# Performance work log

Hardware: AMD Instinct MI355X
Metric: run time of the kernel (lower is better)

The kernel has to match this reference:

```python
import jax, jax.numpy as jnp
import numpy as np
import math

B, T, DM = 2, 2048, 2048
H, D = 16, 128
HALF = D // 2


def _rope_tables(T, half, base=10000.0):
    inv_freq = 1.0 / (base ** (np.arange(0, half, dtype=np.float32) / half))
    t = np.arange(T, dtype=np.float32)
    freqs = np.outer(t, inv_freq)  # [T, half]
    return jnp.asarray(np.cos(freqs)), jnp.asarray(np.sin(freqs))


def setup_inputs() -> dict:
    key = jax.random.key(0)
    ks = jax.random.split(key, 5)
    s = 1.0 / math.sqrt(DM)
    x = jax.random.normal(ks[0], (B, T, DM), dtype=jnp.float32)
    wq = jax.random.normal(ks[1], (H * D, DM), dtype=jnp.float32) * s
    wk = jax.random.normal(ks[2], (H * D, DM), dtype=jnp.float32) * s
    wv = jax.random.normal(ks[3], (H * D, DM), dtype=jnp.float32) * s
    wo = jax.random.normal(ks[4], (DM, H * D), dtype=jnp.float32) * s
    cos, sin = _rope_tables(T, HALF)
    return {"x": x, "wq": wq, "wk": wk, "wv": wv, "wo": wo, "cos": cos, "sin": sin}


def _apply_rope(x, cos, sin):
    # x: [B,H,T,D]; cos/sin: [T, D//2] broadcast over batch and head
    x1, x2 = x[..., :HALF], x[..., HALF:]
    c = cos[None, None]
    s = sin[None, None]
    return jnp.concatenate([x1 * c - x2 * s, x1 * s + x2 * c], axis=-1)


def reference(x, wq, wk, wv, wo, cos, sin):
    Bx, Tx, _ = x.shape
    # QKV projections (Linear with weight [out,in]): y = x @ W^T
    q = jnp.einsum('btd,ed->bte', x, wq).reshape(Bx, Tx, H, D).transpose(0, 2, 1, 3)
    k = jnp.einsum('btd,ed->bte', x, wk).reshape(Bx, Tx, H, D).transpose(0, 2, 1, 3)
    v = jnp.einsum('btd,ed->bte', x, wv).reshape(Bx, Tx, H, D).transpose(0, 2, 1, 3)
    q = _apply_rope(q, cos, sin)
    k = _apply_rope(k, cos, sin)
    # causal SDPA (prefill path: kv_cache=None, mask='causal')
    scale = 1.0 / math.sqrt(D)
    scores = jnp.einsum('bhqd,bhkd->bhqk', q, k) * scale  # [B,H,T,T]
    causal = jnp.tril(jnp.ones((Tx, Tx), dtype=bool))
    scores = jnp.where(causal[None, None], scores, jnp.finfo(scores.dtype).min)
    attn = jax.nn.softmax(scores, axis=-1)
    out = jnp.einsum('bhqk,bhkd->bhqd', attn, v)  # [B,H,T,D]
    out = out.transpose(0, 2, 1, 3).reshape(Bx, Tx, H * D)
    return jnp.einsum('bte,de->btd', out, wo)
```

## Files before the change

### kernel.cpp

```cpp
#include <hip/hip_runtime.h>

typedef __attribute__((ext_vector_type(8))) short short8;
typedef __attribute__((ext_vector_type(4))) float floatx4;

#define B_ 2
#define T_ 2048
#define DM_ 2048
#define H_ 16
#define D_ 128
#define HALF_ 64

__device__ inline unsigned short f2bf(float f) {
    union { float f; unsigned u; } v; v.f = f;
    unsigned r = (v.u + 0x7fffu + ((v.u >> 16) & 1u)) >> 16;
    return (unsigned short)r;
}

__device__ inline void gld16(const void* g, void* l) {
    __builtin_amdgcn_global_load_lds(
        (__attribute__((address_space(1))) void*)g,
        (__attribute__((address_space(3))) void*)l,
        16, 0, 0);
}

__global__ void conv_all(const float* __restrict__ x,
                         const float* __restrict__ w0, const float* __restrict__ w1,
                         const float* __restrict__ w2, const float* __restrict__ w3,
                         unsigned short* __restrict__ xb,
                         unsigned short* __restrict__ wb, int n4w) {
    int y = blockIdx.y;
    int i = blockIdx.x * 256 + threadIdx.x;
    const float* src;
    ushort4* dst;
    if (y < 2) { src = x + (size_t)y * n4w * 4; dst = (ushort4*)xb + (size_t)y * n4w; }
    else {
        src = (y == 2) ? w0 : (y == 3) ? w1 : (y == 4) ? w2 : w3;
        dst = (ushort4*)wb + (size_t)(y - 2) * n4w;
    }
    float4 f = ((const float4*)src)[i];
    ushort4 o;
    o.x = f2bf(f.x); o.y = f2bf(f.y); o.z = f2bf(f.z); o.w = f2bf(f.w);
    dst[i] = o;
}

__global__ __launch_bounds__(256)
void gemm_qkv(const unsigned short* __restrict__ A,
              const unsigned short* __restrict__ W,
              unsigned short* __restrict__ q,
              unsigned short* __restrict__ k,
              unsigned short* __restrict__ vt,
              const float* __restrict__ cosT,
              const float* __restrict__ sinT) {
    __shared__ unsigned short sh[18432];
    unsigned short* As = sh;
    unsigned short* Bs = sh + 8192;

    const int t    = threadIdx.x;
    const int lane = t & 63;
    const int w    = t >> 6;
    const int wm   = w >> 1, wn = w & 1;
    const int l15  = lane & 15, quad = lane >> 4;
    const int bx   = blockIdx.x;
    const int row0 = blockIdx.y * 128;
    const int colg0 = bx * 128;
    const int h     = bx & 15;
    const int K = DM_;

    floatx4 acc[4][4];
    for (int i = 0; i < 4; ++i)
        for (int j = 0; j < 4; ++j)
            acc[i][j] = (floatx4){0.f, 0.f, 0.f, 0.f};

    for (int kt = 0; kt < K / 64; ++kt) {
        if (kt) __syncthreads();
        for (int i = 0; i < 4; ++i) {
            int g  = i * 256 + t;
            int g0 = i * 256 + (t & ~63);
            int m  = g >> 3, c = g & 7;
            int k8 = c ^ (m & 7);
            gld16(A + (size_t)(row0 + m) * K + kt * 64 + k8 * 8, As + (size_t)g0 * 8);
            gld16(W + (size_t)(colg0 + m) * K + kt * 64 + k8 * 8, Bs + (size_t)g0 * 8);
        }
        __syncthreads();

        for (int s = 0; s < 2; ++s) {
            short8 a[4], b[4];
            for (int mf = 0; mf < 4; ++mf) {
                int row = wm * 64 + mf * 16 + l15;
                int pc  = (quad + s * 4) ^ (row & 7);
                a[mf] = *(const short8*)(As + row * 64 + pc * 8);
            }
            for (int nf = 0; nf < 4; ++nf) {
                int row = wn * 32 + (nf & 1) * 16 + (nf >> 1) * 64 + l15;
                int pc  = (quad + s * 4) ^ (row & 7);
                b[nf] = *(const short8*)(Bs + row * 64 + pc * 8);
            }
            for (int mf = 0; mf < 4; ++mf)
                for (int nf = 0; nf < 4; ++nf)
                    acc[mf][nf] = __builtin_amdgcn_mfma_f32_16x16x32_bf16(
                        a[mf], b[nf], acc[mf][nf], 0, 0, 0);
        }
    }

    if (bx < 32) {
        unsigned short* C = (bx < 16) ? q : k;
        for (int mf = 0; mf < 4; ++mf) {
            for (int nf = 0; nf < 2; ++nf) {
                int dh = wn * 32 + nf * 16 + l15;
                for (int r = 0; r < 4; ++r) {
                    int rowg = row0 + wm * 64 + mf * 16 + quad * 4 + r;
                    int tt = rowg & 2047;
                    float c = cosT[tt * 64 + dh];
                    float s = sinT[tt * 64 + dh];
                    float x1 = acc[mf][nf][r];
                    float x2 = acc[mf][nf + 2][r];
                    size_t base = (size_t)rowg * DM_ + h * D_ + dh;
                    C[base]         = f2bf(x1 * c - x2 * s);
                    C[base + HALF_] = f2bf(x1 * s + x2 * c);
                }
            }
        }
    } else {
        __syncthreads();
        unsigned short* P = sh + w * 4608;
        for (int mf = 0; mf < 4; ++mf)
            for (int nf = 0; nf < 4; ++nf) {
                int lc = nf * 16 + l15;
                ushort4 o4;
                o4.x = f2bf(acc[mf][nf][0]); o4.y = f2bf(acc[mf][nf][1]);
                o4.z = f2bf(acc[mf][nf][2]); o4.w = f2bf(acc[mf][nf][3]);
                *(ushort4*)(P + lc * 72 + mf * 16 + quad * 4) = o4;
            }
        __syncthreads();
        const int b  = row0 >> 11;
        const int t0 = (row0 & 2047) + wm * 64;
        for (int it = 0; it < 8; ++it) {
            int cidx = it * 64 + lane;
            int lc = cidx >> 3, t8 = cidx & 7;
            int dh = wn * 32 + ((lc >> 4) & 1) * 16 + (lc >> 5) * 64 + (lc & 15);
            uint4 d = *(const uint4*)(P + lc * 72 + t8 * 8);
            *(uint4*)(vt + ((size_t)(b * 16 + h) * 128 + dh) * T_ + t0 + t8 * 8) = d;
        }
    }
}

__global__ __launch_bounds__(256)
void gemm_bt(const unsigned short* __restrict__ A,
             const unsigned short* __restrict__ W,
             float* __restrict__ C, int M, int N, int K) {
    __shared__ unsigned short As[128 * 64];
    __shared__ unsigned short Bs[128 * 64];

    const int t    = threadIdx.x;
    const int lane = t & 63;
    const int w    = t >> 6;
    const int wm   = w >> 1, wn = w & 1;
    const int l15  = lane & 15, quad = lane >> 4;
    const int row0 = blockIdx.y * 128, col0 = blockIdx.x * 128;

    floatx4 acc[4][4];
    for (int i = 0; i < 4; ++i)
        for (int j = 0; j < 4; ++j)
            acc[i][j] = (floatx4){0.f, 0.f, 0.f, 0.f};

    const int nkt = K >> 6;
    for (int kt = 0; kt < nkt; ++kt) {
        if (kt) __syncthreads();
        for (int i = 0; i < 4; ++i) {
            int g  = i * 256 + t;
            int g0 = i * 256 + (t & ~63);
            int m  = g >> 3, c = g & 7;
            int k8 = c ^ (m & 7);
            gld16(A + (size_t)(row0 + m) * K + kt * 64 + k8 * 8,
                  (unsigned short*)As + (size_t)g0 * 8);
            gld16(W + (size_t)(col0 + m) * K + kt * 64 + k8 * 8,
                  (unsigned short*)Bs + (size_t)g0 * 8);
        }
        __syncthreads();

        for (int s = 0; s < 2; ++s) {
            short8 a[4], b[4];
            for (int mf = 0; mf < 4; ++mf) {
                int row = wm * 64 + mf * 16 + l15;
                int pc  = (quad + s * 4) ^ (row & 7);
                a[mf] = *(const short8*)(As + row * 64 + pc * 8);
            }
            for (int nf = 0; nf < 4; ++nf) {
                int row = wn * 64 + nf * 16 + l15;
                int pc  = (quad + s * 4) ^ (row & 7);
                b[nf] = *(const short8*)(Bs + row * 64 + pc * 8);
            }
            for (int mf = 0; mf < 4; ++mf)
                for (int nf = 0; nf < 4; ++nf)
                    acc[mf][nf] = __builtin_amdgcn_mfma_f32_16x16x32_bf16(
                        a[mf], b[nf], acc[mf][nf], 0, 0, 0);
        }
    }

    for (int mf = 0; mf < 4; ++mf)
        for (int nf = 0; nf < 4; ++nf)
            for (int r = 0; r < 4; ++r) {
                int row = row0 + wm * 64 + mf * 16 + quad * 4 + r;
                int col = col0 + wn * 64 + nf * 16 + l15;
                C[(size_t)row * N + col] = acc[mf][nf][r];
            }
}

__global__ __launch_bounds__(256)
void attn_kernel(const unsigned short* __restrict__ q,
                 const unsigned short* __restrict__ k,
                 const unsigned short* __restrict__ vt,
                 unsigned short* __restrict__ ao) {
    __shared__ unsigned short Ks[64 * 128];
    __shared__ unsigned short Vts[128 * 64];
    __shared__ unsigned short Pw[4][16 * 72];

    const int t    = threadIdx.x;
    const int lane = t & 63, w = t >> 6;
    const int l15  = lane & 15, quad = lane >> 4;
    const int j    = blockIdx.x;
    const int bh   = blockIdx.y;
    const int b    = bh >> 4, h = bh & 15;
    const int qt[2] = {31 - j, j};

    const size_t hoff  = (size_t)h * D_;
    const size_t bbase = (size_t)b * T_ * DM_;

    short8 qa[2][4];
    for (int rs = 0; rs < 2; ++rs) {
        const int qw = qt[rs] * 64 + w * 16;
        const unsigned short* qp = q + bbase + (size_t)(qw + l15) * DM_ + hoff + quad * 8;
        for (int ds = 0; ds < 4; ++ds)
            qa[rs][ds] = *(const short8*)(qp + ds * 32);
    }

    floatx4 o[2][8];
    floatx4 lacc[2];
    for (int rs = 0; rs < 2; ++rs) {
        for (int c = 0; c < 8; ++c) o[rs][c] = (floatx4){0.f, 0.f, 0.f, 0.f};
        lacc[rs] = (floatx4){0.f, 0.f, 0.f, 0.f};
    }
    const unsigned short one_bf = 0x3F80;
    short8 ones;
    for (int i = 0; i < 8; ++i) ones[i] = (short)one_bf;

    const float kS = 0.08838834764831845f;
    const int ktend = qt[0];

    for (int kt = 0; kt <= ktend; ++kt) {
        if (kt) __syncthreads();
        for (int i = 0; i < 4; ++i) {
            int it = w * 4 + i;
            int krow = it * 4 + (lane >> 4);
            int gck  = ((lane & 15) ^ (krow & 7));
            gld16(k + bbase + (size_t)(kt * 64 + krow) * DM_ + hoff + gck * 8,
                  (unsigned short*)Ks + it * 512);
            int vrow = it * 8 + (lane >> 3);
            int gcv  = ((lane & 7) ^ (vrow & 7));
            gld16(vt + ((size_t)bh * 128 + vrow) * T_ + kt * 64 + gcv * 8,
                  (unsigned short*)Vts + it * 512);
        }
        __syncthreads();

        for (int rs = 0; rs < 2; ++rs) {
            const int kd = qt[rs];
            if (kt > kd) continue;
            const int qw = qt[rs] * 64 + w * 16;

            floatx4 s[4];
            for (int f = 0; f < 4; ++f) s[f] = (floatx4){0.f, 0.f, 0.f, 0.f};
            for (int ds = 0; ds < 4; ++ds)
                for (int f = 0; f < 4; ++f) {
                    int krow = f * 16 + l15;
                    int phys = (ds * 4 + quad) ^ (krow & 7);
                    short8 bf = *(const short8*)(Ks + krow * 128 + phys * 8);
                    s[f] = __builtin_amdgcn_mfma_f32_16x16x32_bf16(qa[rs][ds], bf, s[f], 0, 0, 0);
                }

            const bool diag = (kt == kd);
            for (int r = 0; r < 4; ++r) {
                int qrow = qw + quad * 4 + r;
                for (int f = 0; f < 4; ++f) {
                    float x = s[f][r] * kS;
                    float e = __expf(x);
                    if (diag && (kt * 64 + f * 16 + l15 > qrow)) e = 0.f;
                    Pw[w][(quad * 4 + r) * 72 + f * 16 + l15] = f2bf(e);
                }
            }

            short8 pa0 = *(const short8*)(&Pw[w][l15 * 72 + quad * 8]);
            short8 pa1 = *(const short8*)(&Pw[w][l15 * 72 + 32 + quad * 8]);
            lacc[rs] = __builtin_amdgcn_mfma_f32_16x16x32_bf16(pa0, ones, lacc[rs], 0, 0, 0);
            lacc[rs] = __builtin_amdgcn_mfma_f32_16x16x32_bf16(pa1, ones, lacc[rs], 0, 0, 0);
            for (int c = 0; c < 8; ++c) {
                int vrow = c * 16 + l15;
                short8 b0 = *(const short8*)(Vts + vrow * 64 + ((quad) ^ (vrow & 7)) * 8);
                short8 b1 = *(const short8*)(Vts + vrow * 64 + ((4 + quad) ^ (vrow & 7)) * 8);
                o[rs][c] = __builtin_amdgcn_mfma_f32_16x16x32_bf16(pa0, b0, o[rs][c], 0, 0, 0);
                o[rs][c] = __builtin_amdgcn_mfma_f32_16x16x32_bf16(pa1, b1, o[rs][c], 0, 0, 0);
            }
        }
    }

    for (int rs = 0; rs < 2; ++rs) {
        const int qw = qt[rs] * 64 + w * 16;
        for (int r = 0; r < 4; ++r) {
            float inv = 1.0f / lacc[rs][r];
            int qrow = qw + quad * 4 + r;
            size_t obase = bbase + (size_t)qrow * DM_ + hoff;
            for (int c = 0; c < 8; ++c)
                ao[obase + c * 16 + l15] = f2bf(o[rs][c][r] * inv);
        }
    }
}

extern "C" void kernel_launch(void* const* d_in, const int* in_sizes, int n_in,
                              void* d_out, int out_size, void* d_ws, size_t ws_size,
                              hipStream_t stream) {
    const float* x    = (const float*)d_in[0];
    const float* wq   = (const float*)d_in[1];
    const float* wk   = (const float*)d_in[2];
    const float* wv   = (const float*)d_in[3];
    const float* wo   = (const float*)d_in[4];
    const float* cosT = (const float*)d_in[5];
    const float* sinT = (const float*)d_in[6];
    float* out = (float*)d_out;

    const size_t NX = (size_t)B_ * T_ * DM_;
    const size_t NW = (size_t)DM_ * DM_;

    unsigned short* xb  = (unsigned short*)d_ws;
    unsigned short* wqb = xb + NX;
    unsigned short* wob = wqb + 3 * NW;
    unsigned short* qb  = wob + NW;
    unsigned short* kb  = qb + NX;
    unsigned short* vtb = kb + NX;
    unsigned short* aob = vtb + NX;

    conv_all<<<dim3((int)(NW / 4 / 256), 6), 256, 0, stream>>>(
        x, wq, wk, wv, wo, xb, wqb, (int)(NW / 4));

    gemm_qkv<<<dim3(48, 32), 256, 0, stream>>>(xb, wqb, qb, kb, vtb, cosT, sinT);

    attn_kernel<<<dim3(16, B_ * H_), 256, 0, stream>>>(qb, kb, vtb, aob);

    gemm_bt<<<dim3(16, 32), 256, 0, stream>>>(aob, wob, out, B_ * T_, DM_, DM_);
}
```

Before: 356.1 us.

## Rework QKV GEMM into 256x256 tiles with double-buffered phased pipeline

The QKV projection GEMM moves from 128x128 tiles with 256 threads to 256x256 tiles with 512 threads. It double-buffers LDS via direct global-to-LDS loads, interleaving next-tile staging with four MFMA phases per k-step, using explicit barriers, waitcnt and setprio. The goal is to hide global-load latency and raise data reuse per tile. The V-transpose epilogue is rewritten with an XOR-swizzled LDS layout. Costs are a larger LDS footprint (128KB) and fewer blocks (384 vs 1536), which can hurt wave occupancy and tail balance.

New measurement: 375.0 us. +5.3%, slower.

```diff
diff --git a/kernel.cpp b/kernel.cpp
--- a/kernel.cpp
+++ b/kernel.cpp
@@ -43,7 +43,38 @@
     dst[i] = o;
 }
 
-__global__ __launch_bounds__(256)
+
+#define STG(dstoff, srcp, grow0, ii)                                        \
+    { int g_ = (ii) * 512 + t; int m_ = g_ >> 3, c_ = g_ & 7;               \
+      int k8_ = c_ ^ (m_ & 7);                                              \
+      gld16((srcp) + (size_t)((grow0) + m_) * K + (size_t)ktn * 64 + k8_ * 8, \
+            sh + (dstoff) + ((ii) * 512 + (t & ~63)) * 8); }
+
+#define DS_A(PH)                                                            \
+    { _Pragma("unroll") for (int j = 0; j < 2; ++j) {                       \
+        int row_ = (2 * (PH) + j) * 16 + l15;                               \
+        _Pragma("unroll") for (int s = 0; s < 2; ++s) {                     \
+            int pc_ = (quad + s * 4) ^ (row_ & 7);                          \
+            a[j][s] = *(const short8*)(sh + aoff + row_ * 64 + pc_ * 8); } } }
+
+#define MM(PH)                                                              \
+    { _Pragma("unroll") for (int j = 0; j < 2; ++j)                         \
+      _Pragma("unroll") for (int nf = 0; nf < 4; ++nf)                      \
+      _Pragma("unroll") for (int s = 0; s < 2; ++s)                         \
+        acc[2 * (PH) + j][nf] = __builtin_amdgcn_mfma_f32_16x16x32_bf16(    \
+            a[j][s], b[nf][s], acc[2 * (PH) + j][nf], 0, 0, 0); }
+
+#define PHASE_MID()                                                         \
+    __builtin_amdgcn_s_barrier();                                           \
+    asm volatile("s_waitcnt lgkmcnt(0)" ::: "memory");                      \
+    __builtin_amdgcn_sched_barrier(0);                                      \
+    __builtin_amdgcn_s_setprio(1);
+
+#define PHASE_END()                                                         \
+    __builtin_amdgcn_s_setprio(0);                                          \
+    __builtin_amdgcn_s_barrier();
+
+__global__ __launch_bounds__(512, 2)
 void gemm_qkv(const unsigned short* __restrict__ A,
               const unsigned short* __restrict__ W,
               unsigned short* __restrict__ q,
@@ -51,95 +82,143 @@
               unsigned short* __restrict__ vt,
               const float* __restrict__ cosT,
               const float* __restrict__ sinT) {
-    __shared__ unsigned short sh[18432];
-    unsigned short* As = sh;
-    unsigned short* Bs = sh + 8192;
+    __shared__ unsigned short sh[65536];
 
     const int t    = threadIdx.x;
     const int lane = t & 63;
     const int w    = t >> 6;
-    const int wm   = w >> 1, wn = w & 1;
+    const int wm   = w >> 2;
+    const int wn   = w & 3;
+    const int bh   = wn >> 1;
+    const int wodd = wn & 1;
     const int l15  = lane & 15, quad = lane >> 4;
     const int bx   = blockIdx.x;
-    const int row0 = blockIdx.y * 128;
-    const int colg0 = bx * 128;
-    const int h     = bx & 15;
-    const int K = DM_;
-
-    floatx4 acc[4][4];
-    for (int i = 0; i < 4; ++i)
+    const int row0 = blockIdx.y * 256;
+    const int col0 = bx * 256;
+    const int K    = DM_;
+
+    floatx4 acc[8][4];
+#pragma unroll
+    for (int i = 0; i < 8; ++i)
+#pragma unroll
         for (int j = 0; j < 4; ++j)
             acc[i][j] = (floatx4){0.f, 0.f, 0.f, 0.f};
 
-    for (int kt = 0; kt < K / 64; ++kt) {
-        if (kt) __syncthreads();
-        for (int i = 0; i < 4; ++i) {
-            int g  = i * 256 + t;
-            int g0 = i * 256 + (t & ~63);
-            int m  = g >> 3, c = g & 7;
-            int k8 = c ^ (m & 7);
-            gld16(A + (size_t)(row0 + m) * K + kt * 64 + k8 * 8, As + (size_t)g0 * 8);
-            gld16(W + (size_t)(colg0 + m) * K + kt * 64 + k8 * 8, Bs + (size_t)g0 * 8);
-        }
-        __syncthreads();
-
-        for (int s = 0; s < 2; ++s) {
-            short8 a[4], b[4];
-            for (int mf = 0; mf < 4; ++mf) {
-                int row = wm * 64 + mf * 16 + l15;
-                int pc  = (quad + s * 4) ^ (row & 7);
-                a[mf] = *(const short8*)(As + row * 64 + pc * 8);
-            }
-            for (int nf = 0; nf < 4; ++nf) {
-                int row = wn * 32 + (nf & 1) * 16 + (nf >> 1) * 64 + l15;
-                int pc  = (quad + s * 4) ^ (row & 7);
-                b[nf] = *(const short8*)(Bs + row * 64 + pc * 8);
-            }
-            for (int mf = 0; mf < 4; ++mf)
-                for (int nf = 0; nf < 4; ++nf)
-                    acc[mf][nf] = __builtin_amdgcn_mfma_f32_16x16x32_bf16(
-                        a[mf], b[nf], acc[mf][nf], 0, 0, 0);
-        }
-    }
-
-    if (bx < 32) {
-        unsigned short* C = (bx < 16) ? q : k;
-        for (int mf = 0; mf < 4; ++mf) {
+    {
+        const int ktn = 0;
+        STG(32768,        W, col0,       0);
+        STG(32768,        W, col0,       1);
+        STG(32768 + 8192, W, col0 + 128, 0);
+        STG(32768 + 8192, W, col0 + 128, 1);
+        STG(0,            A, row0,       0);
+        STG(8192,         A, row0 + 128, 0);
+        STG(0,            A, row0,       1);
+        STG(8192,         A, row0 + 128, 1);
+    }
+    asm volatile("s_waitcnt vmcnt(2)" ::: "memory");
+    __builtin_amdgcn_s_barrier();
+
+    for (int kt = 0; kt < 32; ++kt) {
+        const int cb   = kt & 1, nb = cb ^ 1;
+        const int ktn  = (kt < 31) ? kt + 1 : 31;
+        const int aoff = cb * 16384 + wm * 8192;
+        const int boff = 32768 + cb * 16384 + bh * 8192;
+        const int nbA  = nb * 16384;
+        const int nbB  = 32768 + nb * 16384;
+        short8 a[2][2];
+        short8 b[4][2];
+
+#pragma unroll
+        for (int nf = 0; nf < 4; ++nf) {
+            int lc = wodd * 32 + (nf & 1) * 16 + (nf >> 1) * 64 + l15;
+#pragma unroll
+            for (int s = 0; s < 2; ++s) {
+                int pc = (quad + s * 4) ^ (lc & 7);
+                b[nf][s] = *(const short8*)(sh + boff + lc * 64 + pc * 8);
+            }
+        }
+        DS_A(0)
+        STG(nbB, W, col0, 0);
+        STG(nbB, W, col0, 1);
+        PHASE_MID()
+        MM(0)
+        PHASE_END()
+
+        DS_A(1)
+        STG(nbB + 8192, W, col0 + 128, 0);
+        STG(nbB + 8192, W, col0 + 128, 1);
+        PHASE_MID()
+        MM(1)
+        __builtin_amdgcn_s_setprio(0);
+        asm volatile("s_waitcnt vmcnt(4)" ::: "memory");
+        __builtin_amdgcn_s_barrier();
+
+        DS_A(2)
+        STG(nbA,        A, row0,       0);
+        STG(nbA + 8192, A, row0 + 128, 0);
+        PHASE_MID()
+        MM(2)
+        PHASE_END()
+
+        DS_A(3)
+        STG(nbA,        A, row0,       1);
+        STG(nbA + 8192, A, row0 + 128, 1);
+        PHASE_MID()
+        MM(3)
+        __builtin_amdgcn_s_setprio(0);
+        asm volatile("s_waitcnt vmcnt(2)" ::: "memory");
+        __builtin_amdgcn_s_barrier();
+    }
+
+    asm volatile("s_waitcnt vmcnt(0)" ::: "memory");
+    __builtin_amdgcn_s_barrier();
+
+    if (bx < 16) {
+        unsigned short* C = (bx < 8) ? q : k;
+        const int hh = ((bx & 7) << 1) + bh;
+#pragma unroll
+        for (int mf = 0; mf < 8; ++mf)
+#pragma unroll
             for (int nf = 0; nf < 2; ++nf) {
-                int dh = wn * 32 + nf * 16 + l15;
+                int dh = wodd * 32 + nf * 16 + l15;
+#pragma unroll
                 for (int r = 0; r < 4; ++r) {
-                    int rowg = row0 + wm * 64 + mf * 16 + quad * 4 + r;
+                    int rowg = row0 + wm * 128 + mf * 16 + quad * 4 + r;
                     int tt = rowg & 2047;
                     float c = cosT[tt * 64 + dh];
                     float s = sinT[tt * 64 + dh];
                     float x1 = acc[mf][nf][r];
                     float x2 = acc[mf][nf + 2][r];
-                    size_t base = (size_t)rowg * DM_ + h * D_ + dh;
+                    size_t base = (size_t)rowg * DM_ + hh * D_ + dh;
                     C[base]         = f2bf(x1 * c - x2 * s);
                     C[base + HALF_] = f2bf(x1 * s + x2 * c);
                 }
             }
-        }
     } else {
-        __syncthreads();
-        unsigned short* P = sh + w * 4608;
-        for (int mf = 0; mf < 4; ++mf)
+#pragma unroll
+        for (int mf = 0; mf < 8; ++mf)
+#pragma unroll
             for (int nf = 0; nf < 4; ++nf) {
-                int lc = nf * 16 + l15;
+                int c  = bh * 128 + wodd * 32 + (nf & 1) * 16 + (nf >> 1) * 64 + l15;
+                int tq = wm * 32 + mf * 4 + quad;
+                int phys = tq ^ ((c & 15) << 2);
                 ushort4 o4;
                 o4.x = f2bf(acc[mf][nf][0]); o4.y = f2bf(acc[mf][nf][1]);
                 o4.z = f2bf(acc[mf][nf][2]); o4.w = f2bf(acc[mf][nf][3]);
-                *(ushort4*)(P + lc * 72 + mf * 16 + quad * 4) = o4;
+                *(ushort4*)(sh + c * 256 + phys * 4) = o4;
             }
         __syncthreads();
-        const int b  = row0 >> 11;
-        const int t0 = (row0 & 2047) + wm * 64;
-        for (int it = 0; it < 8; ++it) {
-            int cidx = it * 64 + lane;
-            int lc = cidx >> 3, t8 = cidx & 7;
-            int dh = wn * 32 + ((lc >> 4) & 1) * 16 + (lc >> 5) * 64 + (lc & 15);
-            uint4 d = *(const uint4*)(P + lc * 72 + t8 * 8);
-            *(uint4*)(vt + ((size_t)(b * 16 + h) * 128 + dh) * T_ + t0 + t8 * 8) = d;
+        const int bb  = row0 >> 11;
+        const int t0g = row0 & 2047;
+        const int hb  = (bx - 16) << 1;
+#pragma unroll
+        for (int i = 0; i < 16; ++i) {
+            int id = i * 512 + t;
+            int c = id >> 5, chk = id & 31;
+            int phys2 = (chk * 2) ^ ((c & 15) << 2);
+            uint4 d = *(const uint4*)(sh + c * 256 + phys2 * 4);
+            int h = hb + (c >> 7), dh = c & 127;
+            *(uint4*)(vt + ((size_t)((bb * 16 + h) * 128 + dh)) * T_ + t0g + chk * 8) = d;
         }
     }
 }
@@ -340,7 +419,7 @@
     conv_all<<<dim3((int)(NW / 4 / 256), 6), 256, 0, stream>>>(
         x, wq, wk, wv, wo, xb, wqb, (int)(NW / 4));
 
-    gemm_qkv<<<dim3(48, 32), 256, 0, stream>>>(xb, wqb, qb, kb, vtb, cosT, sinT);
+    gemm_qkv<<<dim3(24, 16), 512, 0, stream>>>(xb, wqb, qb, kb, vtb, cosT, sinT);
 
     attn_kernel<<<dim3(16, B_ * H_), 256, 0, stream>>>(qb, kb, vtb, aob);
 
```

## Double-buffer QKV GEMM with 128x256 tiles and 512-thread blocks

Applied to the files above, without the earlier changes.

Restructures the fused QKV projection GEMM to use 512-thread blocks computing 128x256 output tiles, with double-buffered LDS staging that prefetches the next K tile while MFMAs run on the current one. It adds explicit barriers, waitcnt and setprio scheduling hints, and rewrites the V-transpose epilogue to use a swizzled LDS layout across the wider tile. The goal is to hide global-load latency and get more A-tile reuse per block. The cost is 96KB of LDS per block, which may limit occupancy, and tighter manual synchronisation.

Result: slower. 371.9 us (+4.4%).

```diff
diff --git a/kernel.cpp b/kernel.cpp
--- a/kernel.cpp
+++ b/kernel.cpp
@@ -43,7 +43,8 @@
     dst[i] = o;
 }
 
-__global__ __launch_bounds__(256)
+
+__global__ __launch_bounds__(512, 2)
 void gemm_qkv(const unsigned short* __restrict__ A,
               const unsigned short* __restrict__ W,
               unsigned short* __restrict__ q,
@@ -51,62 +52,100 @@
               unsigned short* __restrict__ vt,
               const float* __restrict__ cosT,
               const float* __restrict__ sinT) {
-    __shared__ unsigned short sh[18432];
-    unsigned short* As = sh;
-    unsigned short* Bs = sh + 8192;
+    __shared__ unsigned short sh[49152];
 
     const int t    = threadIdx.x;
     const int lane = t & 63;
     const int w    = t >> 6;
-    const int wm   = w >> 1, wn = w & 1;
+    const int wm   = w >> 2;
+    const int wn   = w & 3;
     const int l15  = lane & 15, quad = lane >> 4;
     const int bx   = blockIdx.x;
     const int row0 = blockIdx.y * 128;
-    const int colg0 = bx * 128;
-    const int h     = bx & 15;
-    const int K = DM_;
+    const int col0 = bx * 256;
+    const int K    = DM_;
+    const int browbase = (wn >> 1) * 128 + (wn & 1) * 32;
 
     floatx4 acc[4][4];
+#pragma unroll
     for (int i = 0; i < 4; ++i)
+#pragma unroll
         for (int j = 0; j < 4; ++j)
             acc[i][j] = (floatx4){0.f, 0.f, 0.f, 0.f};
 
-    for (int kt = 0; kt < K / 64; ++kt) {
-        if (kt) __syncthreads();
-        for (int i = 0; i < 4; ++i) {
-            int g  = i * 256 + t;
-            int g0 = i * 256 + (t & ~63);
-            int m  = g >> 3, c = g & 7;
-            int k8 = c ^ (m & 7);
-            gld16(A + (size_t)(row0 + m) * K + kt * 64 + k8 * 8, As + (size_t)g0 * 8);
-            gld16(W + (size_t)(colg0 + m) * K + kt * 64 + k8 * 8, Bs + (size_t)g0 * 8);
-        }
-        __syncthreads();
-
-        for (int s = 0; s < 2; ++s) {
-            short8 a[4], b[4];
-            for (int mf = 0; mf < 4; ++mf) {
-                int row = wm * 64 + mf * 16 + l15;
-                int pc  = (quad + s * 4) ^ (row & 7);
-                a[mf] = *(const short8*)(As + row * 64 + pc * 8);
-            }
-            for (int nf = 0; nf < 4; ++nf) {
-                int row = wn * 32 + (nf & 1) * 16 + (nf >> 1) * 64 + l15;
-                int pc  = (quad + s * 4) ^ (row & 7);
-                b[nf] = *(const short8*)(Bs + row * 64 + pc * 8);
-            }
-            for (int mf = 0; mf < 4; ++mf)
-                for (int nf = 0; nf < 4; ++nf)
-                    acc[mf][nf] = __builtin_amdgcn_mfma_f32_16x16x32_bf16(
-                        a[mf], b[nf], acc[mf][nf], 0, 0, 0);
-        }
-    }
-
-    if (bx < 32) {
-        unsigned short* C = (bx < 16) ? q : k;
-        for (int mf = 0; mf < 4; ++mf) {
+#define STG(dst, srcp, grow)                                                  \
+    { int m_ = t >> 3; int k8_ = (t & 7) ^ (m_ & 7);                          \
+      gld16((srcp) + (size_t)((grow) + m_) * K + ktn * 64 + k8_ * 8,          \
+            sh + (dst) + (t & ~63) * 8); }
+
+#define STAGE_TILE(nb)                                                        \
+    { STG(16384 + (nb) * 16384,         W, col0);                             \
+      STG(16384 + (nb) * 16384 + 4096,  W, col0 + 64);                        \
+      STG(16384 + (nb) * 16384 + 8192,  W, col0 + 128);                       \
+      STG(16384 + (nb) * 16384 + 12288, W, col0 + 192);                       \
+      STG((nb) * 8192,                  A, row0);                             \
+      STG((nb) * 8192 + 4096,           A, row0 + 64); }
+
+#define READ_FRAGS(S)                                                         \
+    { _Pragma("unroll") for (int mf = 0; mf < 4; ++mf) {                      \
+        int row_ = wm * 64 + mf * 16 + l15;                                   \
+        int pc_  = (quad + (S) * 4) ^ (row_ & 7);                             \
+        a[mf] = *(const short8*)(sh + aoff + row_ * 64 + pc_ * 8); }          \
+      _Pragma("unroll") for (int nf = 0; nf < 4; ++nf) {                      \
+        int row_ = browbase + (nf & 1) * 16 + (nf >> 1) * 64 + l15;           \
+        int pc_  = (quad + (S) * 4) ^ (row_ & 7);                             \
+        b[nf] = *(const short8*)(sh + boff + row_ * 64 + pc_ * 8); } }
+
+#define MFMA16()                                                              \
+    { _Pragma("unroll") for (int mf = 0; mf < 4; ++mf)                        \
+      _Pragma("unroll") for (int nf = 0; nf < 4; ++nf)                        \
+        acc[mf][nf] = __builtin_amdgcn_mfma_f32_16x16x32_bf16(                \
+            a[mf], b[nf], acc[mf][nf], 0, 0, 0); }
+
+    {
+        const int ktn = 0;
+        STAGE_TILE(0)
+    }
+    asm volatile("s_waitcnt vmcnt(0)" ::: "memory");
+    __builtin_amdgcn_s_barrier();
+
+    for (int kt = 0; kt < 32; ++kt) {
+        const int cb   = kt & 1, nb = cb ^ 1;
+        const int ktn  = kt + 1;
+        const int aoff = cb * 8192;
+        const int boff = 16384 + cb * 16384;
+        short8 a[4], b[4];
+
+        if (kt < 31) { STAGE_TILE(nb) }
+        READ_FRAGS(0)
+        __builtin_amdgcn_s_barrier();
+        asm volatile("s_waitcnt lgkmcnt(0)" ::: "memory");
+        __builtin_amdgcn_sched_barrier(0);
+        __builtin_amdgcn_s_setprio(1);
+        MFMA16()
+        __builtin_amdgcn_s_setprio(0);
+        __builtin_amdgcn_s_barrier();
+
+        READ_FRAGS(1)
+        __builtin_amdgcn_s_barrier();
+        asm volatile("s_waitcnt lgkmcnt(0)" ::: "memory");
+        __builtin_amdgcn_sched_barrier(0);
+        __builtin_amdgcn_s_setprio(1);
+        MFMA16()
+        __builtin_amdgcn_s_setprio(0);
+        asm volatile("s_waitcnt vmcnt(0)" ::: "memory");
+        __builtin_amdgcn_s_barrier();
+    }
+
+    if (bx < 16) {
+        unsigned short* C = (bx < 8) ? q : k;
+        const int hh = ((bx & 7) << 1) + (wn >> 1);
+#pragma unroll
+        for (int mf = 0; mf < 4; ++mf)
+#pragma unroll
             for (int nf = 0; nf < 2; ++nf) {
-                int dh = wn * 32 + nf * 16 + l15;
+                int dh = (wn & 1) * 32 + nf * 16 + l15;
+#pragma unroll
                 for (int r = 0; r < 4; ++r) {
                     int rowg = row0 + wm * 64 + mf * 16 + quad * 4 + r;
                     int tt = rowg & 2047;
@@ -114,34 +153,43 @@
                     float s = sinT[tt * 64 + dh];
                     float x1 = acc[mf][nf][r];
                     float x2 = acc[mf][nf + 2][r];
-                    size_t base = (size_t)rowg * DM_ + h * D_ + dh;
+                    size_t base = (size_t)rowg * DM_ + hh * D_ + dh;
                     C[base]         = f2bf(x1 * c - x2 * s);
                     C[base + HALF_] = f2bf(x1 * s + x2 * c);
                 }
             }
-        }
     } else {
-        __syncthreads();
-        unsigned short* P = sh + w * 4608;
+#pragma unroll
         for (int mf = 0; mf < 4; ++mf)
+#pragma unroll
             for (int nf = 0; nf < 4; ++nf) {
-                int lc = nf * 16 + l15;
+                int c  = browbase + (nf & 1) * 16 + (nf >> 1) * 64 + l15;
+                int tq = wm * 16 + mf * 4 + quad;
+                int tc = tq >> 1, sub = tq & 1;
+                int ptc = tc ^ (c & 15);
                 ushort4 o4;
                 o4.x = f2bf(acc[mf][nf][0]); o4.y = f2bf(acc[mf][nf][1]);
                 o4.z = f2bf(acc[mf][nf][2]); o4.w = f2bf(acc[mf][nf][3]);
-                *(ushort4*)(P + lc * 72 + mf * 16 + quad * 4) = o4;
+                *(ushort4*)(sh + c * 128 + ptc * 8 + sub * 4) = o4;
             }
         __syncthreads();
-        const int b  = row0 >> 11;
-        const int t0 = (row0 & 2047) + wm * 64;
-        for (int it = 0; it < 8; ++it) {
-            int cidx = it * 64 + lane;
-            int lc = cidx >> 3, t8 = cidx & 7;
-            int dh = wn * 32 + ((lc >> 4) & 1) * 16 + (lc >> 5) * 64 + (lc & 15);
-            uint4 d = *(const uint4*)(P + lc * 72 + t8 * 8);
-            *(uint4*)(vt + ((size_t)(b * 16 + h) * 128 + dh) * T_ + t0 + t8 * 8) = d;
-        }
-    }
+        const int bb  = row0 >> 11;
+        const int t0g = row0 & 2047;
+        const int hb  = (bx - 16) << 1;
+#pragma unroll
+        for (int i = 0; i < 8; ++i) {
+            int id = i * 512 + t;
+            int c = id >> 4, tc = id & 15;
+            int ptc = tc ^ (c & 15);
+            uint4 d = *(const uint4*)(sh + c * 128 + ptc * 8);
+            int h = hb + (c >> 7), dh = c & 127;
+            *(uint4*)(vt + ((size_t)((bb * 16 + h) * 128 + dh)) * T_ + t0g + tc * 8) = d;
+        }
+    }
+#undef STG
+#undef STAGE_TILE
+#undef READ_FRAGS
+#undef MFMA16
 }
 
 __global__ __launch_bounds__(256)
@@ -340,7 +388,7 @@
     conv_all<<<dim3((int)(NW / 4 / 256), 6), 256, 0, stream>>>(
         x, wq, wk, wv, wo, xb, wqb, (int)(NW / 4));
 
-    gemm_qkv<<<dim3(48, 32), 256, 0, stream>>>(xb, wqb, qb, kb, vtb, cosT, sinT);
+    gemm_qkv<<<dim3(24, 32), 512, 0, stream>>>(xb, wqb, qb, kb, vtb, cosT, sinT);
 
     attn_kernel<<<dim3(16, B_ * H_), 256, 0, stream>>>(qb, kb, vtb, aob);
 
```

## Read K and V directly from global memory in attention, dropping LDS staging

Applied to the files above, without the earlier changes.

Removes the shared-memory staging of K and V tiles, together with its two block-wide barriers per key tile. Each wave now loads its MFMA B operands straight from global memory and relies on L1/L2 caching for reuse across the four waves. MFMA sections are wrapped in s_setprio to raise wave priority. This gives up explicit data sharing in LDS and latency hiding via barriers, so redundant global traffic and exposed load latency may grow.

Result: slower. 533.9 us (+49.9%).

```diff
diff --git a/kernel.cpp b/kernel.cpp
--- a/kernel.cpp
+++ b/kernel.cpp
@@ -211,8 +211,6 @@
                  const unsigned short* __restrict__ k,
                  const unsigned short* __restrict__ vt,
                  unsigned short* __restrict__ ao) {
-    __shared__ unsigned short Ks[64 * 128];
-    __shared__ unsigned short Vts[128 * 64];
     __shared__ unsigned short Pw[4][16 * 72];
 
     const int t    = threadIdx.x;
@@ -247,21 +245,10 @@
     const float kS = 0.08838834764831845f;
     const int ktend = qt[0];
 
+    const unsigned short* kb0 = k + bbase + hoff;
+    const unsigned short* vb0 = vt + (size_t)bh * 128 * T_;
+
     for (int kt = 0; kt <= ktend; ++kt) {
-        if (kt) __syncthreads();
-        for (int i = 0; i < 4; ++i) {
-            int it = w * 4 + i;
-            int krow = it * 4 + (lane >> 4);
-            int gck  = ((lane & 15) ^ (krow & 7));
-            gld16(k + bbase + (size_t)(kt * 64 + krow) * DM_ + hoff + gck * 8,
-                  (unsigned short*)Ks + it * 512);
-            int vrow = it * 8 + (lane >> 3);
-            int gcv  = ((lane & 7) ^ (vrow & 7));
-            gld16(vt + ((size_t)bh * 128 + vrow) * T_ + kt * 64 + gcv * 8,
-                  (unsigned short*)Vts + it * 512);
-        }
-        __syncthreads();
-
         for (int rs = 0; rs < 2; ++rs) {
             const int kd = qt[rs];
             if (kt > kd) continue;
@@ -269,17 +256,25 @@
 
             floatx4 s[4];
             for (int f = 0; f < 4; ++f) s[f] = (floatx4){0.f, 0.f, 0.f, 0.f};
-            for (int ds = 0; ds < 4; ++ds)
-                for (int f = 0; f < 4; ++f) {
-                    int krow = f * 16 + l15;
-                    int phys = (ds * 4 + quad) ^ (krow & 7);
-                    short8 bf = *(const short8*)(Ks + krow * 128 + phys * 8);
-                    s[f] = __builtin_amdgcn_mfma_f32_16x16x32_bf16(qa[rs][ds], bf, s[f], 0, 0, 0);
+            __builtin_amdgcn_s_setprio(1);
+#pragma unroll
+            for (int f = 0; f < 4; ++f) {
+                const unsigned short* kp =
+                    kb0 + (size_t)(kt * 64 + f * 16 + l15) * DM_ + quad * 8;
+#pragma unroll
+                for (int ds = 0; ds < 4; ++ds) {
+                    short8 bf = *(const short8*)(kp + ds * 32);
+                    s[f] = __builtin_amdgcn_mfma_f32_16x16x32_bf16(
+                        qa[rs][ds], bf, s[f], 0, 0, 0);
                 }
+            }
+            __builtin_amdgcn_s_setprio(0);
 
             const bool diag = (kt == kd);
+#pragma unroll
             for (int r = 0; r < 4; ++r) {
                 int qrow = qw + quad * 4 + r;
+#pragma unroll
                 for (int f = 0; f < 4; ++f) {
                     float x = s[f][r] * kS;
                     float e = __expf(x);
@@ -292,13 +287,18 @@
             short8 pa1 = *(const short8*)(&Pw[w][l15 * 72 + 32 + quad * 8]);
             lacc[rs] = __builtin_amdgcn_mfma_f32_16x16x32_bf16(pa0, ones, lacc[rs], 0, 0, 0);
             lacc[rs] = __builtin_amdgcn_mfma_f32_16x16x32_bf16(pa1, ones, lacc[rs], 0, 0, 0);
+
+            __builtin_amdgcn_s_setprio(1);
+#pragma unroll
             for (int c = 0; c < 8; ++c) {
-                int vrow = c * 16 + l15;
-                short8 b0 = *(const short8*)(Vts + vrow * 64 + ((quad) ^ (vrow & 7)) * 8);
-                short8 b1 = *(const short8*)(Vts + vrow * 64 + ((4 + quad) ^ (vrow & 7)) * 8);
+                const unsigned short* vp =
+                    vb0 + (size_t)(c * 16 + l15) * T_ + kt * 64 + quad * 8;
+                short8 b0 = *(const short8*)(vp);
+                short8 b1 = *(const short8*)(vp + 32);
                 o[rs][c] = __builtin_amdgcn_mfma_f32_16x16x32_bf16(pa0, b0, o[rs][c], 0, 0, 0);
                 o[rs][c] = __builtin_amdgcn_mfma_f32_16x16x32_bf16(pa1, b1, o[rs][c], 0, 0, 0);
             }
+            __builtin_amdgcn_s_setprio(0);
         }
     }
 
```
